# Kernel tuning notes

Hardware: AMD Instinct MI355X
Metric: run time of the kernel (lower is better)

The kernel has to match this reference:

```python
import jax, jax.numpy as jnp
import numpy as np
from jax import lax

E = 300      # _embsize
H = 32       # attention heads
ADIM = 64    # projection_dim (attention and values dim)
FF = 100     # feedforward hidden dim
NK = 11      # gaussian kernels
NCONV = 5    # conv kernel sizes 1..5
COUT = 16    # conv out channels for k>=2

def _kernel_mus(n):
    l = [1.0]
    b = 2.0 / (n - 1)
    l.append(1 - b / 2)
    for i in range(1, n - 1):
        l.append(l[i] - b)
    return l

def _kernel_sigmas(n):
    b = 2.0 / (n - 1)
    return [0.0001] + [0.5 * b] * (n - 1)

MU = jnp.asarray(_kernel_mus(NK), jnp.float32).reshape(1, 1, 1, 1, NK)
SIG = jnp.asarray(_kernel_sigmas(NK), jnp.float32).reshape(1, 1, 1, 1, NK)

def _pos_features(T, d):
    # allennlp add_positional_features, min_timescale=1, max_timescale=1e4, d even
    nt = d // 2
    inv = np.exp(np.arange(nt, dtype=np.float32) * -(np.log(1e4) / (nt - 1)))
    pos = np.arange(T, dtype=np.float32)[:, None] * inv[None, :]
    return jnp.asarray(np.concatenate([np.sin(pos), np.cos(pos)], axis=1))

def _layer_norm(x, g, b, eps=1e-6):
    m = jnp.mean(x, -1, keepdims=True)
    s = jnp.std(x, -1, keepdims=True)  # biased std, as allennlp LayerNorm
    return g * (x - m) / (s + eps) + b

def _mhsa(x, mask, Wc, bc, Wo, bo):
    # allennlp MultiHeadSelfAttention: combined projection, scale=sqrt(input_dim//heads)
    B, T, _ = x.shape
    comb = x @ Wc + bc                                   # [B,T,3*ADIM]
    q, k, v = comb[..., :ADIM], comb[..., ADIM:2 * ADIM], comb[..., 2 * ADIM:]
    dh = ADIM // H
    split = lambda t: t.reshape(B, T, H, dh).transpose(0, 2, 1, 3)
    q, k, v = split(q), split(k), split(v)
    scale = float(np.sqrt(E // H))
    sim = jnp.einsum('bhqd,bhkd->bhqk', q / scale, k)
    m = mask[:, None, None, :]
    p = jax.nn.softmax(sim * m, axis=-1) * m             # old allennlp masked_softmax
    p = p / (jnp.sum(p, -1, keepdims=True) + 1e-13)
    o = jnp.einsum('bhqk,bhkd->bhqd', p, v).transpose(0, 2, 1, 3).reshape(B, T, ADIM)
    return o @ Wo + bo

def _encode(x, mask, W1, b1, W2, b2, ffg, ffb, Wc, bc, Wo, bo, lng, lnb):
    # StackedSelfAttentionEncoder, 1 layer, all dropouts = 0
    out = x + _pos_features(x.shape[1], E)[None]
    ff = jax.nn.relu(out @ W1 + b1) @ W2 + b2
    ff = _layer_norm(ff + out, ffg, ffb)                 # residual (dims match)
    att = _mhsa(ff, mask, Wc, bc, Wo, bo)
    return _layer_norm(att + ff, lng, lnb)

def _conv(x, w, b, k):
    if k > 1:
        x = jnp.pad(x, ((0, 0), (0, 0), (0, k - 1), (0, k - 1)))  # ConstantPad2d(0,k-1,0,k-1)
    y = lax.conv_general_dilated(x, w, (1, 1), 'VALID',
                                 dimension_numbers=('NCHW', 'OIHW', 'NCHW'))
    y = y + b[None, :, None, None]
    if k > 1:
        y = jnp.max(y, axis=1, keepdims=True)            # MaxPool3d over channel dim
    return y

def setup_inputs() -> dict:
    key = jax.random.key(0)
    ks = iter(jax.random.split(key, 40))
    B, Q, D = 16, 32, 512
    nrm = lambda shape, s=0.05: jax.random.normal(next(ks), shape, jnp.float32) * s
    return {
        'query_embeddings': jax.random.normal(next(ks), (B, Q, E), jnp.float32),
        'document_embeddings': jax.random.normal(next(ks), (B, D, E), jnp.float32),
        'query_pad_oov_mask': jnp.ones((B, Q), jnp.float32),
        'document_pad_oov_mask': jnp.ones((B, D), jnp.float32),
        'query_idfs': jax.random.uniform(next(ks), (B, Q, 1), jnp.float32),
        'document_idfs': jax.random.uniform(next(ks), (B, D, 1), jnp.float32),
        'W1': nrm((E, FF)), 'b1': jnp.zeros((FF,), jnp.float32),
        'W2': nrm((FF, E)), 'b2': jnp.zeros((E,), jnp.float32),
        'ffg': jnp.ones((E,), jnp.float32), 'ffb': jnp.zeros((E,), jnp.float32),
        'Wc': nrm((E, 3 * ADIM)), 'bc': jnp.zeros((3 * ADIM,), jnp.float32),
        'Wo': nrm((ADIM, E)), 'bo': jnp.zeros((E,), jnp.float32),
        'lng': jnp.ones((E,), jnp.float32), 'lnb': jnp.zeros((E,), jnp.float32),
        'c1w': nrm((1, 2, 1, 1)), 'c1b': jnp.zeros((1,), jnp.float32),
        'c2w': nrm((COUT, 2, 2, 2)), 'c2b': jnp.zeros((COUT,), jnp.float32),
        'c3w': nrm((COUT, 2, 3, 3)), 'c3b': jnp.zeros((COUT,), jnp.float32),
        'c4w': nrm((COUT, 2, 4, 4)), 'c4b': jnp.zeros((COUT,), jnp.float32),
        'c5w': nrm((COUT, 2, 5, 5)), 'c5b': jnp.zeros((COUT,), jnp.float32),
        'dw': nrm((1, NK * NCONV)), 'db': jnp.zeros((1,), jnp.float32),
        'dmw': nrm((1, NK * NCONV)), 'dmb': jnp.zeros((1,), jnp.float32),
        'cw': nrm((1, 2)),
    }

def reference(query_embeddings, document_embeddings, query_pad_oov_mask,
              document_pad_oov_mask, query_idfs, document_idfs,
              W1, b1, W2, b2, ffg, ffb, Wc, bc, Wo, bo, lng, lnb,
              c1w, c1b, c2w, c2b, c3w, c3b, c4w, c4b, c5w, c5b,
              dw, db, dmw, dmb, cw):
    qm, dmask = query_pad_oov_mask, document_pad_oov_mask
    enc = lambda x, m: _encode(x, m, W1, b1, W2, b2, ffg, ffb, Wc, bc, Wo, bo, lng, lnb)
    q_ctx = enc(query_embeddings, qm) * qm[..., None]
    d_ctx = enc(document_embeddings, dmask) * dmask[..., None]
    # cosine on raw embeddings, dot product on contextualized
    qn = query_embeddings / (jnp.linalg.norm(query_embeddings, axis=-1, keepdims=True) + 1e-13)
    dn = document_embeddings / (jnp.linalg.norm(document_embeddings, axis=-1, keepdims=True) + 1e-13)
    cos = jnp.einsum('bqe,bde->bqd', qn, dn)[:, None]
    dot = jnp.einsum('bqe,bde->bqd', q_ctx, d_ctx)[:, None]
    combined = jnp.tanh(jnp.concatenate([cos, dot], axis=1))     # [B,2,Q,D]
    convs = [_conv(combined, w, b, k) for k, (w, b) in enumerate(
        [(c1w, c1b), (c2w, c2b), (c3w, c3b), (c4w, c4b), (c5w, c5b)], start=1)]
    all_conv = jnp.concatenate(convs, axis=1)[..., None]         # [B,5,Q,D,1]
    qd_mask = (qm[:, :, None] * dmask[:, None, :])[:, None, :, :, None]  # [B,1,Q,D,1]
    raw = jnp.exp(-(all_conv - MU) ** 2 / (2.0 * SIG ** 2))      # [B,5,Q,D,NK]
    masked = raw * qd_mask
    doc_len = jnp.sum(dmask, 1)                                  # [B]
    pkq = jnp.sum(masked, axis=3)                                # [B,5,Q,NK]
    log_pkq = jnp.log(jnp.clip(pkq, 1e-10, None)) * qm[:, None, :, None]
    per_kernel = jnp.sum(log_pkq, axis=2)                        # [B,5,NK]
    pkq_mean = pkq / doc_len[:, None, None, None]
    log_pkq_mean = jnp.log(jnp.clip(pkq_mean, 1e-10, None)) * qm[:, None, :, None]
    per_kernel_mean = jnp.sum(log_pkq_mean, axis=2)
    B = per_kernel.shape[0]
    d1 = per_kernel.reshape(B, -1) @ dw.T + db
    d2 = per_kernel_mean.reshape(B, -1) @ dmw.T + dmb
    return (jnp.concatenate([d1, d2], axis=1) @ cw.T)[:, 0]
```

## Files before the change

kernel.cpp:

```cpp
#include <hip/hip_runtime.h>

namespace {

constexpr int E_  = 300;
constexpr int FF_ = 100;
constexpr int AD_ = 64;
constexpr int NH_ = 32;
constexpr int CD_ = 192;
constexpr int B_  = 16;
constexpr int TQ_ = 32;
constexpr int TD_ = 512;
constexpr int NK_ = 11;
constexpr int DOCBLK_ = 512;

__device__ __forceinline__ float wave_sum(float v) {
#pragma unroll
  for (int o = 32; o > 0; o >>= 1) v += __shfl_down(v, o);
  return v;
}

__device__ __forceinline__ int swz16(int e, int t) {
  return e * 16 + (t ^ (((e >> 2) & 7) << 1));
}

__device__ __forceinline__ void fma4(float4& a, float s, const float4& w) {
  a.x = fmaf(s, w.x, a.x); a.y = fmaf(s, w.y, a.y);
  a.z = fmaf(s, w.z, a.z); a.w = fmaf(s, w.w, a.w);
}

__device__ __forceinline__ void gl_lds16(const float4* g, float4* l) {
  __builtin_amdgcn_global_load_lds(
      (const __attribute__((address_space(1))) void*)g,
      (__attribute__((address_space(3))) void*)l, 16, 0, 0);
}

__device__ __forceinline__ void stage_chunk(const float4* __restrict__ src,
                                            float4* __restrict__ dst,
                                            int n, int tid) {
  for (int j = tid; j < n; j += 256) gl_lds16(src + j, dst + j);
}

__global__ __launch_bounds__(256)
void encode_front_v5(const float* __restrict__ qe, const float* __restrict__ de,
                     const float* __restrict__ W1, const float* __restrict__ b1,
                     const float* __restrict__ W2, const float* __restrict__ b2,
                     const float* __restrict__ ffg, const float* __restrict__ ffb,
                     const float* __restrict__ Wc, const float* __restrict__ bc,
                     float* __restrict__ ffq, float* __restrict__ combq,
                     float* __restrict__ qn,
                     float* __restrict__ ffd, float* __restrict__ combd,
                     float* __restrict__ dnT)
{
  __shared__ float  s_A[4800];
  __shared__ float  s_h1[1600];
  __shared__ float4 s_w[2][1500];
  __shared__ float  s_stat[16][17];
  __shared__ float  s_norm[16];

  const int tid = threadIdx.x;
  const int ct = tid & 31, tg = tid >> 5;
  const int t0 = tg * 2;
  const bool doc = (blockIdx.x < DOCBLK_);
  const int sb = doc ? blockIdx.x : (blockIdx.x - DOCBLK_);
  const float* xs = (doc ? de : qe) + (size_t)sb * 16 * E_;
  float* ffo = doc ? ffd : ffq;
  float* cmo = doc ? combd : combq;
  const size_t tok0 = (size_t)sb * 16;
  const int bb_ = doc ? (int)(tok0 >> 9) : (int)(tok0 >> 5);
  const int tp0 = doc ? (int)(tok0 & 511) : (int)(tok0 & 31);

  const float4* W1f4 = (const float4*)W1;
  const float4* W2f4 = (const float4*)W2;
  const float4* Wcf4 = (const float4*)Wc;

  stage_chunk(W1f4, &s_w[0][0], 1500, tid);

  for (int i = tid; i < 1200; i += 256) {
    const float4 v = *(const float4*)(xs + (size_t)i * 4);
    const int t = i / 75, e0 = (i % 75) * 4;
    s_A[swz16(e0 + 0, t)] = v.x; s_A[swz16(e0 + 1, t)] = v.y;
    s_A[swz16(e0 + 2, t)] = v.z; s_A[swz16(e0 + 3, t)] = v.w;
  }
  __syncthreads();
  {
    const int tk = tid & 15, ch = tid >> 4;
    const int kb = ch * 19, ke = (kb + 19 < 300) ? kb + 19 : 300;
    float ss = 0.f;
    for (int k = kb; k < ke; ++k) { const float v = s_A[swz16(k, tk)]; ss = fmaf(v, v, ss); }
    s_stat[ch][tk] = ss;
  }
  __syncthreads();
  if (tid < 16) {
    float s = 0.f;
#pragma unroll
    for (int i = 0; i < 16; ++i) s += s_stat[i][tid];
    s_norm[tid] = 1.f / (sqrtf(s) + 1e-13f);
  }
  __syncthreads();
  for (int i = tid; i < 1200; i += 256) {
    const int t = i / 75, e0 = (i % 75) * 4;
    const int tp = tp0 + t;
    const float nm = s_norm[t];
#pragma unroll
    for (int j = 0; j < 4; ++j) {
      const int e = e0 + j;
      const int slot = swz16(e, t);
      const float raw = s_A[slot];
      if (doc) dnT[((size_t)bb_ * E_ + e) * 512 + tp] = raw * nm;
      else     qn[(tok0 + t) * E_ + e] = raw * nm;
      const int f = (e < 150) ? e : e - 150;
      const float ang = __expf(-0.061814365f * (float)f) * (float)tp;
      s_A[slot] = raw + ((e < 150) ? sinf(ang) : cosf(ang));
    }
  }
  __syncthreads();

  {
    const int cq = (ct < 25) ? ct : 24;
    float4 a1[2];
    a1[0] = make_float4(0.f, 0.f, 0.f, 0.f);
    a1[1] = make_float4(0.f, 0.f, 0.f, 0.f);
    for (int c = 0; c < 5; ++c) {
      if (c < 4) stage_chunk(W1f4 + 1500 * (c + 1), &s_w[(c + 1) & 1][0], 1500, tid);
      else       stage_chunk(W2f4,                  &s_w[1][0],           1500, tid);
      const float4* wb = &s_w[c & 1][0];
#pragma unroll 6
      for (int kk = 0; kk < 60; ++kk) {
        const float2 xv = *(const float2*)&s_A[swz16(c * 60 + kk, t0)];
        const float4 w = wb[kk * 25 + cq];
        fma4(a1[0], xv.x, w); fma4(a1[1], xv.y, w);
      }
      if (c == 4 && ct < 25) {
        const float4 bb = *(const float4*)&b1[4 * ct];
#pragma unroll
        for (int r = 0; r < 2; ++r) {
          const int t = t0 + r;
          const float4 a = (r == 0) ? a1[0] : a1[1];
          s_h1[swz16(4 * ct + 0, t)] = fmaxf(a.x + bb.x, 0.f);
          s_h1[swz16(4 * ct + 1, t)] = fmaxf(a.y + bb.y, 0.f);
          s_h1[swz16(4 * ct + 2, t)] = fmaxf(a.z + bb.z, 0.f);
          s_h1[swz16(4 * ct + 3, t)] = fmaxf(a.w + bb.w, 0.f);
        }
      }
      __syncthreads();
    }
  }

  {
    const int q2 = (ct < 11) ? ct + 64 : 74;
    const bool val2 = (ct < 11);
    float4 a2[3][2];
#pragma unroll
    for (int p = 0; p < 3; ++p)
#pragma unroll
      for (int r = 0; r < 2; ++r) a2[p][r] = make_float4(0.f, 0.f, 0.f, 0.f);
    for (int c = 0; c < 5; ++c) {
      if (c < 4) stage_chunk(W2f4 + 1500 * (c + 1), &s_w[c & 1][0], 1500, tid);
      else       stage_chunk(Wcf4,                  &s_w[0][0],     1440, tid);
      const float4* wb = &s_w[(c + 1) & 1][0];
#pragma unroll 5
      for (int kk = 0; kk < 20; ++kk) {
        const float2 hv = *(const float2*)&s_h1[swz16(c * 20 + kk, t0)];
        const float4 w0 = wb[kk * 75 + ct];
        const float4 w1 = wb[kk * 75 + ct + 32];
        const float4 w2 = wb[kk * 75 + q2];
        fma4(a2[0][0], hv.x, w0); fma4(a2[0][1], hv.y, w0);
        fma4(a2[1][0], hv.x, w1); fma4(a2[1][1], hv.y, w1);
        fma4(a2[2][0], hv.x, w2); fma4(a2[2][1], hv.y, w2);
      }
      if (c == 4) {
        float sum[2] = {0.f, 0.f}, sq[2] = {0.f, 0.f};
#pragma unroll
        for (int p = 0; p < 3; ++p) {
          const int qq = (p == 0) ? ct : (p == 1) ? ct + 32 : q2;
          const bool ok = (p < 2) || val2;
          if (!ok) break;
          const float4 bb = *(const float4*)&b2[4 * qq];
#pragma unroll
          for (int r = 0; r < 2; ++r) {
            const int t = t0 + r;
            float4 v = a2[p][r];
            v.x += bb.x + s_A[swz16(4 * qq + 0, t)];
            v.y += bb.y + s_A[swz16(4 * qq + 1, t)];
            v.z += bb.z + s_A[swz16(4 * qq + 2, t)];
            v.w += bb.w + s_A[swz16(4 * qq + 3, t)];
            a2[p][r] = v;
            sum[r] += v.x + v.y + v.z + v.w;
            sq[r] = fmaf(v.x, v.x, fmaf(v.y, v.y, fmaf(v.z, v.z, fmaf(v.w, v.w, sq[r]))));
          }
        }
#pragma unroll
        for (int m = 1; m <= 16; m <<= 1) {
#pragma unroll
          for (int r = 0; r < 2; ++r) {
            sum[r] += __shfl_xor(sum[r], m);
            sq[r]  += __shfl_xor(sq[r], m);
          }
        }
#pragma unroll
        for (int r = 0; r < 2; ++r) {
          const int t = t0 + r;
          const float mean = sum[r] * (1.f / 300.f);
          const float var  = fmaxf(sq[r] * (1.f / 300.f) - mean * mean, 0.f);
          const float rstd = 1.f / (sqrtf(var) + 1e-6f);
#pragma unroll
          for (int p = 0; p < 3; ++p) {
            if (p == 2 && !val2) break;
            const int qq = (p == 0) ? ct : (p == 1) ? ct + 32 : q2;
            const int c0 = 4 * qq;
            const float4 g4 = *(const float4*)&ffg[c0];
            const float4 b4 = *(const float4*)&ffb[c0];
            const float4 v = a2[p][r];
            float4 fv;
            fv.x = fmaf(g4.x, (v.x - mean) * rstd, b4.x);
            fv.y = fmaf(g4.y, (v.y - mean) * rstd, b4.y);
            fv.z = fmaf(g4.z, (v.z - mean) * rstd, b4.z);
            fv.w = fmaf(g4.w, (v.w - mean) * rstd, b4.w);
            *(float4*)&ffo[(tok0 + t) * E_ + c0] = fv;
            s_A[swz16(c0 + 0, t)] = fv.x; s_A[swz16(c0 + 1, t)] = fv.y;
            s_A[swz16(c0 + 2, t)] = fv.z; s_A[swz16(c0 + 3, t)] = fv.w;
          }
        }
      }
      __syncthreads();
    }
  }

  {
    const int q3 = (ct < 16) ? ct + 32 : 47;
    float4 a3[2][2];
#pragma unroll
    for (int p = 0; p < 2; ++p)
#pragma unroll
      for (int r = 0; r < 2; ++r) a3[p][r] = make_float4(0.f, 0.f, 0.f, 0.f);
    for (int c = 0; c < 10; ++c) {
      if (c < 9) stage_chunk(Wcf4 + 1440 * (c + 1), &s_w[(c + 1) & 1][0], 1440, tid);
      const float4* wb = &s_w[c & 1][0];
#pragma unroll 6
      for (int kk = 0; kk < 30; ++kk) {
        const float2 xv = *(const float2*)&s_A[swz16(c * 30 + kk, t0)];
        const float4 w0 = wb[kk * 48 + ct];
        const float4 w1 = wb[kk * 48 + q3];
        fma4(a3[0][0], xv.x, w0); fma4(a3[0][1], xv.y, w0);
        fma4(a3[1][0], xv.x, w1); fma4(a3[1][1], xv.y, w1);
      }
      if (c < 9) __syncthreads();
    }
    const float4 bb0 = *(const float4*)&bc[4 * ct];
#pragma unroll
    for (int r = 0; r < 2; ++r) {
      float4 o = a3[0][r];
      o.x += bb0.x; o.y += bb0.y; o.z += bb0.z; o.w += bb0.w;
      *(float4*)&cmo[(tok0 + t0 + r) * CD_ + 4 * ct] = o;
    }
    if (ct < 16) {
      const float4 bb1 = *(const float4*)&bc[4 * (ct + 32)];
#pragma unroll
      for (int r = 0; r < 2; ++r) {
        float4 o = a3[1][r];
        o.x += bb1.x; o.y += bb1.y; o.z += bb1.z; o.w += bb1.w;
        *(float4*)&cmo[(tok0 + t0 + r) * CD_ + 4 * (ct + 32)] = o;
      }
    }
  }
}

template <int T>
__global__ __launch_bounds__(512)
void attn(const float* __restrict__ comb, const float* __restrict__ mask,
          float* __restrict__ o)
{
  __shared__ float4 s_kv[T];
  __shared__ float  s_m[T];
  const int bh = blockIdx.x, b = bh / NH_, h = bh % NH_;
  const int tid = threadIdx.x;
  const float* cb = comb + (size_t)b * T * CD_;
  if (tid < T) {
    const float* c = cb + (size_t)tid * CD_;
    const float m = mask[b * T + tid];
    s_kv[tid] = make_float4(c[AD_ + 2 * h] * m, c[AD_ + 2 * h + 1] * m,
                            c[2 * AD_ + 2 * h], c[2 * AD_ + 2 * h + 1]);
    s_m[tid] = m;
  }
  __syncthreads();
  if (tid < T) {
    const float* c = cb + (size_t)tid * CD_;
    const float q0 = c[2 * h] * (1.f / 3.f);
    const float q1 = c[2 * h + 1] * (1.f / 3.f);
    float M = -1e30f;
    for (int j = 0; j < T; ++j) {
      const float4 kv = s_kv[j];
      M = fmaxf(M, fmaf(q0, kv.x, q1 * kv.y));
    }
    float S = 0.f, W = 0.f, a0 = 0.f, a1 = 0.f;
    for (int j = 0; j < T; ++j) {
      const float4 kv = s_kv[j];
      const float s = fmaf(q0, kv.x, q1 * kv.y);
      const float z = __expf(s - M);
      const float w = z * s_m[j];
      S += z; W += w;
      a0 = fmaf(w, kv.z, a0);
      a1 = fmaf(w, kv.w, a1);
    }
    const float dn = 1.f / (W + 1e-13f * S);
    float* op = o + (size_t)(b * T + tid) * AD_ + 2 * h;
    op[0] = a0 * dn;
    op[1] = a1 * dn;
  }
}

__global__ __launch_bounds__(256)
void encode_back_v3(const float* __restrict__ oq, const float* __restrict__ od,
                    const float* __restrict__ ffq, const float* __restrict__ ffd,
                    const float* __restrict__ Wo, const float* __restrict__ bo,
                    const float* __restrict__ lng, const float* __restrict__ lnb,
                    const float* __restrict__ qm, const float* __restrict__ dm,
                    float* __restrict__ qctx, float* __restrict__ dctxT)
{
  __shared__ float  s_O[1024];
  __shared__ float4 s_w[2][1200];

  const int tid = threadIdx.x;
  const int ct = tid & 31, tg = tid >> 5;
  const int t0 = tg * 2;
  const bool doc = (blockIdx.x < DOCBLK_);
  const int sb = doc ? blockIdx.x : (blockIdx.x - DOCBLK_);
  const size_t tok0 = (size_t)sb * 16;
  const float* op = doc ? od : oq;
  const float* ffp = doc ? ffd : ffq;
  const float* mp = doc ? dm : qm;
  const int bb_ = doc ? (int)(tok0 >> 9) : 0;
  const int tp0 = doc ? (int)(tok0 & 511) : 0;

  const float4* Wof4 = (const float4*)Wo;
  stage_chunk(Wof4, &s_w[0][0], 1200, tid);

  {
    const int t = tid >> 4, c0 = (tid & 15) * 4;
    const float4 v = *(const float4*)(op + (tok0 + t) * AD_ + c0);
    s_O[swz16(c0 + 0, t)] = v.x; s_O[swz16(c0 + 1, t)] = v.y;
    s_O[swz16(c0 + 2, t)] = v.z; s_O[swz16(c0 + 3, t)] = v.w;
  }
  __syncthreads();

  const int q2 = (ct < 11) ? ct + 64 : 74;
  const bool val2 = (ct < 11);
  float4 a[3][2];
#pragma unroll
  for (int p = 0; p < 3; ++p)
#pragma unroll
    for (int r = 0; r < 2; ++r) a[p][r] = make_float4(0.f, 0.f, 0.f, 0.f);
  for (int c = 0; c < 4; ++c) {
    if (c < 3) stage_chunk(Wof4 + 1200 * (c + 1), &s_w[(c + 1) & 1][0], 1200, tid);
    const float4* wb = &s_w[c & 1][0];
#pragma unroll 4
    for (int kk = 0; kk < 16; ++kk) {
      const float2 ov = *(const float2*)&s_O[swz16(c * 16 + kk, t0)];
      const float4 w0 = wb[kk * 75 + ct];
      const float4 w1 = wb[kk * 75 + ct + 32];
      const float4 w2 = wb[kk * 75 + q2];
      fma4(a[0][0], ov.x, w0); fma4(a[0][1], ov.y, w0);
      fma4(a[1][0], ov.x, w1); fma4(a[1][1], ov.y, w1);
      fma4(a[2][0], ov.x, w2); fma4(a[2][1], ov.y, w2);
    }
    if (c < 3) __syncthreads();
  }
  float sum[2] = {0.f, 0.f}, sq[2] = {0.f, 0.f};
#pragma unroll
  for (int p = 0; p < 3; ++p) {
    const int qq = (p == 0) ? ct : (p == 1) ? ct + 32 : q2;
    const bool ok = (p < 2) || val2;
    if (!ok) break;
    const float4 bb = *(const float4*)&bo[4 * qq];
#pragma unroll
    for (int r = 0; r < 2; ++r) {
      const int t = t0 + r;
      const float4 f4 = *(const float4*)(ffp + (tok0 + t) * E_ + 4 * qq);
      float4 v = a[p][r];
      v.x += bb.x + f4.x; v.y += bb.y + f4.y;
      v.z += bb.z + f4.z; v.w += bb.w + f4.w;
      a[p][r] = v;
      sum[r] += v.x + v.y + v.z + v.w;
      sq[r] = fmaf(v.x, v.x, fmaf(v.y, v.y, fmaf(v.z, v.z, fmaf(v.w, v.w, sq[r]))));
    }
  }
#pragma unroll
  for (int m = 1; m <= 16; m <<= 1) {
#pragma unroll
    for (int r = 0; r < 2; ++r) {
      sum[r] += __shfl_xor(sum[r], m);
      sq[r]  += __shfl_xor(sq[r], m);
    }
  }
#pragma unroll
  for (int r = 0; r < 2; ++r) {
    const int t = t0 + r;
    const float mean = sum[r] * (1.f / 300.f);
    const float var  = fmaxf(sq[r] * (1.f / 300.f) - mean * mean, 0.f);
    const float rstd = 1.f / (sqrtf(var) + 1e-6f);
    const float mk = mp[tok0 + t];
#pragma unroll
    for (int p = 0; p < 3; ++p) {
      if (p == 2 && !val2) break;
      const int qq = (p == 0) ? ct : (p == 1) ? ct + 32 : q2;
      const int c0 = 4 * qq;
      const float4 g4 = *(const float4*)&lng[c0];
      const float4 b4 = *(const float4*)&lnb[c0];
      const float4 v = a[p][r];
      float4 fv;
      fv.x = fmaf(g4.x, (v.x - mean) * rstd, b4.x) * mk;
      fv.y = fmaf(g4.y, (v.y - mean) * rstd, b4.y) * mk;
      fv.z = fmaf(g4.z, (v.z - mean) * rstd, b4.z) * mk;
      fv.w = fmaf(g4.w, (v.w - mean) * rstd, b4.w) * mk;
      if (doc) {
        const int tp = tp0 + t;
        dctxT[((size_t)bb_ * E_ + c0 + 0) * 512 + tp] = fv.x;
        dctxT[((size_t)bb_ * E_ + c0 + 1) * 512 + tp] = fv.y;
        dctxT[((size_t)bb_ * E_ + c0 + 2) * 512 + tp] = fv.z;
        dctxT[((size_t)bb_ * E_ + c0 + 3) * 512 + tp] = fv.w;
      } else {
        *(float4*)&qctx[(tok0 + t) * E_ + c0] = fv;
      }
    }
  }
}

__global__ __launch_bounds__(512)
void simtanh_v2(const float* __restrict__ qctx, const float* __restrict__ qn,
                const float* __restrict__ dctxT, const float* __restrict__ dnT,
                float* __restrict__ combined)
{
  __shared__ float s_q[2 * 16 * 304];
  __shared__ float s_part[8 * 32 * 64];

  const int bid = blockIdx.x;
  const int sub = bid & 15, b = bid >> 4;
  const int qh = sub >> 3, dc = sub & 7;
  const int tid = threadIdx.x;
  const int ep = tid >> 6, dlane = tid & 63;
  const int d = dc * 64 + dlane;

  const float* qc  = qctx + ((size_t)b * 32 + qh * 16) * E_;
  const float* qnp = qn   + ((size_t)b * 32 + qh * 16) * E_;
  for (int i = tid; i < 1200; i += 512) {
    const int q = i / 75, e0 = (i % 75) * 4;
    *(float4*)&s_q[(0 * 16 + q) * 304 + e0] = *(const float4*)(qc + q * E_ + e0);
    *(float4*)&s_q[(1 * 16 + q) * 304 + e0] = *(const float4*)(qnp + q * E_ + e0);
  }
  __syncthreads();

  const float* dct = dctxT + (size_t)b * E_ * 512 + d;
  const float* dnt = dnT   + (size_t)b * E_ * 512 + d;
  float accD[16], accC[16];
#pragma unroll
  for (int q = 0; q < 16; ++q) { accD[q] = 0.f; accC[q] = 0.f; }
  const int es = ep * 40, ee = (es + 40 < 300) ? es + 40 : 300;
  for (int e0 = es; e0 < ee; e0 += 4) {
    const float dv0 = dct[(size_t)(e0 + 0) * 512];
    const float dv1 = dct[(size_t)(e0 + 1) * 512];
    const float dv2 = dct[(size_t)(e0 + 2) * 512];
    const float dv3 = dct[(size_t)(e0 + 3) * 512];
    const float dn0 = dnt[(size_t)(e0 + 0) * 512];
    const float dn1 = dnt[(size_t)(e0 + 1) * 512];
    const float dn2 = dnt[(size_t)(e0 + 2) * 512];
    const float dn3 = dnt[(size_t)(e0 + 3) * 512];
#pragma unroll
    for (int q = 0; q < 16; ++q) {
      const float4 qd = *(const float4*)&s_q[(0 * 16 + q) * 304 + e0];
      const float4 qc4 = *(const float4*)&s_q[(1 * 16 + q) * 304 + e0];
      float aD = accD[q], aC = accC[q];
      aD = fmaf(qd.x, dv0, aD); aD = fmaf(qd.y, dv1, aD);
      aD = fmaf(qd.z, dv2, aD); aD = fmaf(qd.w, dv3, aD);
      aC = fmaf(qc4.x, dn0, aC); aC = fmaf(qc4.y, dn1, aC);
      aC = fmaf(qc4.z, dn2, aC); aC = fmaf(qc4.w, dn3, aC);
      accD[q] = aD; accC[q] = aC;
    }
  }
#pragma unroll
  for (int q = 0; q < 16; ++q) {
    s_part[(ep * 32 + q * 2 + 0) * 64 + dlane] = accC[q];
    s_part[(ep * 32 + q * 2 + 1) * 64 + dlane] = accD[q];
  }
  __syncthreads();
  const int s0 = (tid >> 6) * 4;
#pragma unroll
  for (int si = 0; si < 4; ++si) {
    const int s = s0 + si;
    float v = 0.f;
#pragma unroll
    for (int p = 0; p < 8; ++p) v += s_part[(p * 32 + s) * 64 + dlane];
    const int q = s >> 1, typ = s & 1;
    combined[(((size_t)b * 2 + typ) * 32 + qh * 16 + q) * 512 + d] = tanhf(v);
  }
}

template <int K>
__device__ __forceinline__ float conv_max16(const float* __restrict__ s_in, int j,
                                            const float* __restrict__ w,
                                            const float* __restrict__ bias)
{
  float patch[2][K][K];
#pragma unroll
  for (int c = 0; c < 2; ++c)
#pragma unroll
    for (int di = 0; di < K; ++di)
#pragma unroll
      for (int dj = 0; dj < K; ++dj)
        patch[c][di][dj] = s_in[(c * 5 + di) * 516 + j + dj];
  float best = -1e30f;
#pragma unroll
  for (int oc = 0; oc < 16; ++oc) {
    float acc = bias[oc];
#pragma unroll
    for (int c = 0; c < 2; ++c)
#pragma unroll
      for (int di = 0; di < K; ++di)
#pragma unroll
        for (int dj = 0; dj < K; ++dj)
          acc = fmaf(patch[c][di][dj], w[((oc * 2 + c) * K + di) * K + dj], acc);
    best = fmaxf(best, acc);
  }
  return best;
}

__global__ __launch_bounds__(512)
void conv_all(const float* __restrict__ combined,
              const float* __restrict__ c1w, const float* __restrict__ c1b,
              const float* __restrict__ c2w, const float* __restrict__ c2b,
              const float* __restrict__ c3w, const float* __restrict__ c3b,
              const float* __restrict__ c4w, const float* __restrict__ c4b,
              const float* __restrict__ c5w, const float* __restrict__ c5b,
              float* __restrict__ convout)
{
  __shared__ float s_in[2 * 5 * 516];
  __shared__ float s_w[1730];
  __shared__ float s_b[66];
  const int blk = blockIdx.x, b = blk >> 5, i = blk & 31;
  const int tid = threadIdx.x;
  for (int idx = tid; idx < 2 * 5 * 516; idx += 512) {
    const int c = idx / (5 * 516), rem = idx % (5 * 516), r = rem / 516, j = rem % 516;
    const int row = i + r;
    float v = 0.f;
    if (row < 32 && j < 512)
      v = combined[((size_t)(b * 2 + c) * 32 + row) * 512 + j];
    s_in[idx] = v;
  }
  if (tid < 2)   s_w[tid] = c1w[tid];
  if (tid < 128) s_w[2 + tid] = c2w[tid];
  if (tid < 288) s_w[130 + tid] = c3w[tid];
  s_w[418 + tid] = c4w[tid];
  for (int idx = tid; idx < 800; idx += 512) s_w[930 + idx] = c5w[idx];
  if (tid == 0) s_b[0] = c1b[0];
  if (tid < 16) {
    s_b[1 + tid]  = c2b[tid];
    s_b[17 + tid] = c3b[tid];
    s_b[33 + tid] = c4b[tid];
    s_b[49 + tid] = c5b[tid];
  }
  __syncthreads();
  const int j = tid;
  const float o1 = fmaf(s_in[j], s_w[0], fmaf(s_in[5 * 516 + j], s_w[1], s_b[0]));
  convout[((size_t)(b * 5 + 0) * 32 + i) * 512 + j] = o1;
  convout[((size_t)(b * 5 + 1) * 32 + i) * 512 + j] = conv_max16<2>(s_in, j, s_w + 2,   s_b + 1);
  convout[((size_t)(b * 5 + 2) * 32 + i) * 512 + j] = conv_max16<3>(s_in, j, s_w + 130, s_b + 17);
  convout[((size_t)(b * 5 + 3) * 32 + i) * 512 + j] = conv_max16<4>(s_in, j, s_w + 418, s_b + 33);
  convout[((size_t)(b * 5 + 4) * 32 + i) * 512 + j] = conv_max16<5>(s_in, j, s_w + 930, s_b + 49);
}

__global__ __launch_bounds__(512)
void rbf_pkq(const float* __restrict__ convout, const float* __restrict__ dmask,
             const float* __restrict__ qmask, float* __restrict__ pkq)
{
  __shared__ float red[8][NK_];
  const int id = blockIdx.x;
  const int q = id & 31;
  const int b = id / 160;
  const int tid = threadIdx.x;
  const float x = convout[(size_t)id * 512 + tid];
  const float dmv = dmask[b * 512 + tid];
  const float mu[NK_]  = {1.f, .9f, .7f, .5f, .3f, .1f, -.1f, -.3f, -.5f, -.7f, -.9f};
  const float nis[NK_] = {-5e7f, -50.f, -50.f, -50.f, -50.f, -50.f,
                          -50.f, -50.f, -50.f, -50.f, -50.f};
  const int lane = tid & 63, w = tid >> 6;
#pragma unroll
  for (int k = 0; k < NK_; ++k) {
    const float df = x - mu[k];
    float v = __expf(df * df * nis[k]) * dmv;
    v = wave_sum(v);
    if (lane == 0) red[w][k] = v;
  }
  __syncthreads();
  if (tid < NK_) {
    float s = 0.f;
#pragma unroll
    for (int ww = 0; ww < 8; ++ww) s += red[ww][tid];
    pkq[(size_t)id * NK_ + tid] = s * qmask[b * 32 + q];
  }
}

__global__ __launch_bounds__(64)
void final_k(const float* __restrict__ pkq, const float* __restrict__ qmask,
             const float* __restrict__ dmask,
             const float* __restrict__ dw, const float* __restrict__ db,
             const float* __restrict__ dmw, const float* __restrict__ dmb,
             const float* __restrict__ cw, float* __restrict__ out)
{
  const int b = blockIdx.x, tid = threadIdx.x;
  float dl = 0.f;
  for (int j = tid; j < 512; j += 64) dl += dmask[b * 512 + j];
  dl = wave_sum(dl);
  dl = __shfl(dl, 0);
  float v1 = 0.f, v2 = 0.f;
  if (tid < 55) {
    const int c = tid / NK_, k = tid % NK_;
    const float rdl = 1.f / dl;
    float s1 = 0.f, s2 = 0.f;
    for (int q = 0; q < 32; ++q) {
      const float p = pkq[(size_t)((b * 5 + c) * 32 + q) * NK_ + k];
      const float qmv = qmask[b * 32 + q];
      s1 += logf(fmaxf(p, 1e-10f)) * qmv;
      s2 += logf(fmaxf(p * rdl, 1e-10f)) * qmv;
    }
    v1 = s1 * dw[tid];
    v2 = s2 * dmw[tid];
  }
  v1 = wave_sum(v1);
  v2 = wave_sum(v2);
  if (tid == 0) out[b] = (v1 + db[0]) * cw[0] + (v2 + dmb[0]) * cw[1];
}

}

extern "C" void kernel_launch(void* const* d_in, const int* in_sizes, int n_in,
                              void* d_out, int out_size, void* d_ws, size_t ws_size,
                              hipStream_t stream)
{
  const float* qe  = (const float*)d_in[0];
  const float* de  = (const float*)d_in[1];
  const float* qm  = (const float*)d_in[2];
  const float* dm  = (const float*)d_in[3];
  const float* W1  = (const float*)d_in[6];
  const float* b1  = (const float*)d_in[7];
  const float* W2  = (const float*)d_in[8];
  const float* b2  = (const float*)d_in[9];
  const float* ffg = (const float*)d_in[10];
  const float* ffb = (const float*)d_in[11];
  const float* Wc  = (const float*)d_in[12];
  const float* bc  = (const float*)d_in[13];
  const float* Wo  = (const float*)d_in[14];
  const float* bo  = (const float*)d_in[15];
  const float* lng = (const float*)d_in[16];
  const float* lnb = (const float*)d_in[17];
  const float* c1w = (const float*)d_in[18];
  const float* c1b = (const float*)d_in[19];
  const float* c2w = (const float*)d_in[20];
  const float* c2b = (const float*)d_in[21];
  const float* c3w = (const float*)d_in[22];
  const float* c3b = (const float*)d_in[23];
  const float* c4w = (const float*)d_in[24];
  const float* c4b = (const float*)d_in[25];
  const float* c5w = (const float*)d_in[26];
  const float* c5b = (const float*)d_in[27];
  const float* dwp  = (const float*)d_in[28];
  const float* dbp  = (const float*)d_in[29];
  const float* dmwp = (const float*)d_in[30];
  const float* dmbp = (const float*)d_in[31];
  const float* cwp  = (const float*)d_in[32];

  float* ws = (float*)d_ws;
  size_t off = 0;
  auto alloc = [&](size_t n) { float* p = ws + off; off += n; return p; };
  float* ffq      = alloc((size_t)B_ * TQ_ * E_);
  float* combq    = alloc((size_t)B_ * TQ_ * CD_);
  float* oq       = alloc((size_t)B_ * TQ_ * AD_);
  float* qctx     = alloc((size_t)B_ * TQ_ * E_);
  float* qn       = alloc((size_t)B_ * TQ_ * E_);
  float* ffd      = alloc((size_t)B_ * TD_ * E_);
  float* combd    = alloc((size_t)B_ * TD_ * CD_);
  float* od       = alloc((size_t)B_ * TD_ * AD_);
  float* dctxT    = alloc((size_t)B_ * E_ * TD_);
  float* dnT      = alloc((size_t)B_ * E_ * TD_);
  float* combined = alloc((size_t)B_ * 2 * TQ_ * TD_);
  float* convout  = alloc((size_t)B_ * 5 * TQ_ * TD_);
  float* pkq      = alloc((size_t)B_ * 5 * TQ_ * NK_);

  encode_front_v5<<<DOCBLK_ + 32, 256, 0, stream>>>(
      qe, de, W1, b1, W2, b2, ffg, ffb, Wc, bc,
      ffq, combq, qn, ffd, combd, dnT);
  attn<TQ_><<<B_ * NH_, 64, 0, stream>>>(combq, qm, oq);
  attn<TD_><<<B_ * NH_, 512, 0, stream>>>(combd, dm, od);
  encode_back_v3<<<DOCBLK_ + 32, 256, 0, stream>>>(
      oq, od, ffq, ffd, Wo, bo, lng, lnb, qm, dm, qctx, dctxT);
  simtanh_v2<<<256, 512, 0, stream>>>(qctx, qn, dctxT, dnT, combined);
  conv_all<<<B_ * 32, 512, 0, stream>>>(
      combined, c1w, c1b, c2w, c2b, c3w, c3b, c4w, c4b, c5w, c5b, convout);
  rbf_pkq<<<B_ * 5 * TQ_, 512, 0, stream>>>(convout, dm, qm, pkq);
  final_k<<<B_, 64, 0, stream>>>(pkq, qm, dm, dwp, dbp, dmwp, dmbp, cwp,
                                 (float*)d_out);
}
```

Measured before the change: 382.0 us.

## Read encoder weights directly from global memory instead of LDS double-buffering

Removes the global_load_lds double-buffered staging of W1, W2, Wc and Wo in the encode front and back kernels. Weight rows are now read straight from global memory (through the caches) inside single flat k-loops, with no per-chunk barriers. This cuts LDS usage per block, which can raise occupancy, and drops many __syncthreads, but each thread now waits on global/L2 latency for weights that used to be prefetched.

After: 415.8 us. 8.8% more time.

```diff
diff --git a/kernel.cpp b/kernel.cpp
--- a/kernel.cpp
+++ b/kernel.cpp
@@ -28,20 +28,8 @@
   a.z = fmaf(s, w.z, a.z); a.w = fmaf(s, w.w, a.w);
 }
 
-__device__ __forceinline__ void gl_lds16(const float4* g, float4* l) {
-  __builtin_amdgcn_global_load_lds(
-      (const __attribute__((address_space(1))) void*)g,
-      (__attribute__((address_space(3))) void*)l, 16, 0, 0);
-}
-
-__device__ __forceinline__ void stage_chunk(const float4* __restrict__ src,
-                                            float4* __restrict__ dst,
-                                            int n, int tid) {
-  for (int j = tid; j < n; j += 256) gl_lds16(src + j, dst + j);
-}
-
 __global__ __launch_bounds__(256)
-void encode_front_v5(const float* __restrict__ qe, const float* __restrict__ de,
+void encode_front_v6(const float* __restrict__ qe, const float* __restrict__ de,
                      const float* __restrict__ W1, const float* __restrict__ b1,
                      const float* __restrict__ W2, const float* __restrict__ b2,
                      const float* __restrict__ ffg, const float* __restrict__ ffb,
@@ -51,11 +39,10 @@
                      float* __restrict__ ffd, float* __restrict__ combd,
                      float* __restrict__ dnT)
 {
-  __shared__ float  s_A[4800];
-  __shared__ float  s_h1[1600];
-  __shared__ float4 s_w[2][1500];
-  __shared__ float  s_stat[16][17];
-  __shared__ float  s_norm[16];
+  __shared__ float s_A[4800];
+  __shared__ float s_h1[1600];
+  __shared__ float s_stat[16][17];
+  __shared__ float s_norm[16];
 
   const int tid = threadIdx.x;
   const int ct = tid & 31, tg = tid >> 5;
@@ -73,8 +60,6 @@
   const float4* W2f4 = (const float4*)W2;
   const float4* Wcf4 = (const float4*)Wc;
 
-  stage_chunk(W1f4, &s_w[0][0], 1500, tid);
-
   for (int i = tid; i < 1200; i += 256) {
     const float4 v = *(const float4*)(xs + (size_t)i * 4);
     const int t = i / 75, e0 = (i % 75) * 4;
@@ -120,30 +105,25 @@
     float4 a1[2];
     a1[0] = make_float4(0.f, 0.f, 0.f, 0.f);
     a1[1] = make_float4(0.f, 0.f, 0.f, 0.f);
-    for (int c = 0; c < 5; ++c) {
-      if (c < 4) stage_chunk(W1f4 + 1500 * (c + 1), &s_w[(c + 1) & 1][0], 1500, tid);
-      else       stage_chunk(W2f4,                  &s_w[1][0],           1500, tid);
-      const float4* wb = &s_w[c & 1][0];
-#pragma unroll 6
-      for (int kk = 0; kk < 60; ++kk) {
-        const float2 xv = *(const float2*)&s_A[swz16(c * 60 + kk, t0)];
-        const float4 w = wb[kk * 25 + cq];
-        fma4(a1[0], xv.x, w); fma4(a1[1], xv.y, w);
+#pragma unroll 10
+    for (int k = 0; k < 300; ++k) {
+      const float2 xv = *(const float2*)&s_A[swz16(k, t0)];
+      const float4 w = W1f4[k * 25 + cq];
+      fma4(a1[0], xv.x, w); fma4(a1[1], xv.y, w);
+    }
+    if (ct < 25) {
+      const float4 bb = *(const float4*)&b1[4 * ct];
+#pragma unroll
+      for (int r = 0; r < 2; ++r) {
+        const int t = t0 + r;
+        const float4 a = (r == 0) ? a1[0] : a1[1];
+        s_h1[swz16(4 * ct + 0, t)] = fmaxf(a.x + bb.x, 0.f);
+        s_h1[swz16(4 * ct + 1, t)] = fmaxf(a.y + bb.y, 0.f);
+        s_h1[swz16(4 * ct + 2, t)] = fmaxf(a.z + bb.z, 0.f);
+        s_h1[swz16(4 * ct + 3, t)] = fmaxf(a.w + bb.w, 0.f);
       }
-      if (c == 4 && ct < 25) {
-        const float4 bb = *(const float4*)&b1[4 * ct];
-#pragma unroll
-        for (int r = 0; r < 2; ++r) {
-          const int t = t0 + r;
-          const float4 a = (r == 0) ? a1[0] : a1[1];
-          s_h1[swz16(4 * ct + 0, t)] = fmaxf(a.x + bb.x, 0.f);
-          s_h1[swz16(4 * ct + 1, t)] = fmaxf(a.y + bb.y, 0.f);
-          s_h1[swz16(4 * ct + 2, t)] = fmaxf(a.z + bb.z, 0.f);
-          s_h1[swz16(4 * ct + 3, t)] = fmaxf(a.w + bb.w, 0.f);
-        }
-      }
-      __syncthreads();
-    }
+    }
+    __syncthreads();
   }
 
   {
@@ -154,76 +134,69 @@
     for (int p = 0; p < 3; ++p)
 #pragma unroll
       for (int r = 0; r < 2; ++r) a2[p][r] = make_float4(0.f, 0.f, 0.f, 0.f);
-    for (int c = 0; c < 5; ++c) {
-      if (c < 4) stage_chunk(W2f4 + 1500 * (c + 1), &s_w[c & 1][0], 1500, tid);
-      else       stage_chunk(Wcf4,                  &s_w[0][0],     1440, tid);
-      const float4* wb = &s_w[(c + 1) & 1][0];
 #pragma unroll 5
-      for (int kk = 0; kk < 20; ++kk) {
-        const float2 hv = *(const float2*)&s_h1[swz16(c * 20 + kk, t0)];
-        const float4 w0 = wb[kk * 75 + ct];
-        const float4 w1 = wb[kk * 75 + ct + 32];
-        const float4 w2 = wb[kk * 75 + q2];
-        fma4(a2[0][0], hv.x, w0); fma4(a2[0][1], hv.y, w0);
-        fma4(a2[1][0], hv.x, w1); fma4(a2[1][1], hv.y, w1);
-        fma4(a2[2][0], hv.x, w2); fma4(a2[2][1], hv.y, w2);
+    for (int k = 0; k < 100; ++k) {
+      const float2 hv = *(const float2*)&s_h1[swz16(k, t0)];
+      const float4 w0 = W2f4[k * 75 + ct];
+      const float4 w1 = W2f4[k * 75 + ct + 32];
+      const float4 w2 = W2f4[k * 75 + q2];
+      fma4(a2[0][0], hv.x, w0); fma4(a2[0][1], hv.y, w0);
+      fma4(a2[1][0], hv.x, w1); fma4(a2[1][1], hv.y, w1);
+      fma4(a2[2][0], hv.x, w2); fma4(a2[2][1], hv.y, w2);
+    }
+    float sum[2] = {0.f, 0.f}, sq[2] = {0.f, 0.f};
+#pragma unroll
+    for (int p = 0; p < 3; ++p) {
+      const int qq = (p == 0) ? ct : (p == 1) ? ct + 32 : q2;
+      const bool ok = (p < 2) || val2;
+      if (!ok) break;
+      const float4 bb = *(const float4*)&b2[4 * qq];
+#pragma unroll
+      for (int r = 0; r < 2; ++r) {
+        const int t = t0 + r;
+        float4 v = a2[p][r];
+        v.x += bb.x + s_A[swz16(4 * qq + 0, t)];
+        v.y += bb.y + s_A[swz16(4 * qq + 1, t)];
+        v.z += bb.z + s_A[swz16(4 * qq + 2, t)];
+        v.w += bb.w + s_A[swz16(4 * qq + 3, t)];
+        a2[p][r] = v;
+        sum[r] += v.x + v.y + v.z + v.w;
+        sq[r] = fmaf(v.x, v.x, fmaf(v.y, v.y, fmaf(v.z, v.z, fmaf(v.w, v.w, sq[r]))));
       }
-      if (c == 4) {
-        float sum[2] = {0.f, 0.f}, sq[2] = {0.f, 0.f};
-#pragma unroll
-        for (int p = 0; p < 3; ++p) {
-          const int qq = (p == 0) ? ct : (p == 1) ? ct + 32 : q2;
-          const bool ok = (p < 2) || val2;
-          if (!ok) break;
-          const float4 bb = *(const float4*)&b2[4 * qq];
-#pragma unroll
-          for (int r = 0; r < 2; ++r) {
-            const int t = t0 + r;
-            float4 v = a2[p][r];
-            v.x += bb.x + s_A[swz16(4 * qq + 0, t)];
-            v.y += bb.y + s_A[swz16(4 * qq + 1, t)];
-            v.z += bb.z + s_A[swz16(4 * qq + 2, t)];
-            v.w += bb.w + s_A[swz16(4 * qq + 3, t)];
-            a2[p][r] = v;
-            sum[r] += v.x + v.y + v.z + v.w;
-            sq[r] = fmaf(v.x, v.x, fmaf(v.y, v.y, fmaf(v.z, v.z, fmaf(v.w, v.w, sq[r]))));
-          }
-        }
-#pragma unroll
-        for (int m = 1; m <= 16; m <<= 1) {
-#pragma unroll
-          for (int r = 0; r < 2; ++r) {
-            sum[r] += __shfl_xor(sum[r], m);
-            sq[r]  += __shfl_xor(sq[r], m);
-          }
-        }
-#pragma unroll
-        for (int r = 0; r < 2; ++r) {
-          const int t = t0 + r;
-          const float mean = sum[r] * (1.f / 300.f);
-          const float var  = fmaxf(sq[r] * (1.f / 300.f) - mean * mean, 0.f);
-          const float rstd = 1.f / (sqrtf(var) + 1e-6f);
-#pragma unroll
-          for (int p = 0; p < 3; ++p) {
-            if (p == 2 && !val2) break;
-            const int qq = (p == 0) ? ct : (p == 1) ? ct + 32 : q2;
-            const int c0 = 4 * qq;
-            const float4 g4 = *(const float4*)&ffg[c0];
-            const float4 b4 = *(const float4*)&ffb[c0];
-            const float4 v = a2[p][r];
-            float4 fv;
-            fv.x = fmaf(g4.x, (v.x - mean) * rstd, b4.x);
-            fv.y = fmaf(g4.y, (v.y - mean) * rstd, b4.y);
-            fv.z = fmaf(g4.z, (v.z - mean) * rstd, b4.z);
-            fv.w = fmaf(g4.w, (v.w - mean) * rstd, b4.w);
-            *(float4*)&ffo[(tok0 + t) * E_ + c0] = fv;
-            s_A[swz16(c0 + 0, t)] = fv.x; s_A[swz16(c0 + 1, t)] = fv.y;
-            s_A[swz16(c0 + 2, t)] = fv.z; s_A[swz16(c0 + 3, t)] = fv.w;
-          }
-        }
+    }
+#pragma unroll
+    for (int m = 1; m <= 16; m <<= 1) {
+#pragma unroll
+      for (int r = 0; r < 2; ++r) {
+        sum[r] += __shfl_xor(sum[r], m);
+        sq[r]  += __shfl_xor(sq[r], m);
       }
-      __syncthreads();
-    }
+    }
+#pragma unroll
+    for (int r = 0; r < 2; ++r) {
+      const int t = t0 + r;
+      const float mean = sum[r] * (1.f / 300.f);
+      const float var  = fmaxf(sq[r] * (1.f / 300.f) - mean * mean, 0.f);
+      const float rstd = 1.f / (sqrtf(var) + 1e-6f);
+#pragma unroll
+      for (int p = 0; p < 3; ++p) {
+        if (p == 2 && !val2) break;
+        const int qq = (p == 0) ? ct : (p == 1) ? ct + 32 : q2;
+        const int c0 = 4 * qq;
+        const float4 g4 = *(const float4*)&ffg[c0];
+        const float4 b4 = *(const float4*)&ffb[c0];
+        const float4 v = a2[p][r];
+        float4 fv;
+        fv.x = fmaf(g4.x, (v.x - mean) * rstd, b4.x);
+        fv.y = fmaf(g4.y, (v.y - mean) * rstd, b4.y);
+        fv.z = fmaf(g4.z, (v.z - mean) * rstd, b4.z);
+        fv.w = fmaf(g4.w, (v.w - mean) * rstd, b4.w);
+        *(float4*)&ffo[(tok0 + t) * E_ + c0] = fv;
+        s_A[swz16(c0 + 0, t)] = fv.x; s_A[swz16(c0 + 1, t)] = fv.y;
+        s_A[swz16(c0 + 2, t)] = fv.z; s_A[swz16(c0 + 3, t)] = fv.w;
+      }
+    }
+    __syncthreads();
   }
 
   {
@@ -233,18 +206,13 @@
     for (int p = 0; p < 2; ++p)
 #pragma unroll
       for (int r = 0; r < 2; ++r) a3[p][r] = make_float4(0.f, 0.f, 0.f, 0.f);
-    for (int c = 0; c < 10; ++c) {
-      if (c < 9) stage_chunk(Wcf4 + 1440 * (c + 1), &s_w[(c + 1) & 1][0], 1440, tid);
-      const float4* wb = &s_w[c & 1][0];
-#pragma unroll 6
-      for (int kk = 0; kk < 30; ++kk) {
-        const float2 xv = *(const float2*)&s_A[swz16(c * 30 + kk, t0)];
-        const float4 w0 = wb[kk * 48 + ct];
-        const float4 w1 = wb[kk * 48 + q3];
-        fma4(a3[0][0], xv.x, w0); fma4(a3[0][1], xv.y, w0);
-        fma4(a3[1][0], xv.x, w1); fma4(a3[1][1], xv.y, w1);
-      }
-      if (c < 9) __syncthreads();
+#pragma unroll 10
+    for (int k = 0; k < 300; ++k) {
+      const float2 xv = *(const float2*)&s_A[swz16(k, t0)];
+      const float4 w0 = Wcf4[k * 48 + ct];
+      const float4 w1 = Wcf4[k * 48 + q3];
+      fma4(a3[0][0], xv.x, w0); fma4(a3[0][1], xv.y, w0);
+      fma4(a3[1][0], xv.x, w1); fma4(a3[1][1], xv.y, w1);
     }
     const float4 bb0 = *(const float4*)&bc[4 * ct];
 #pragma unroll
@@ -310,15 +278,14 @@
 }
 
 __global__ __launch_bounds__(256)
-void encode_back_v3(const float* __restrict__ oq, const float* __restrict__ od,
+void encode_back_v4(const float* __restrict__ oq, const float* __restrict__ od,
                     const float* __restrict__ ffq, const float* __restrict__ ffd,
                     const float* __restrict__ Wo, const float* __restrict__ bo,
                     const float* __restrict__ lng, const float* __restrict__ lnb,
                     const float* __restrict__ qm, const float* __restrict__ dm,
                     float* __restrict__ qctx, float* __restrict__ dctxT)
 {
-  __shared__ float  s_O[1024];
-  __shared__ float4 s_w[2][1200];
+  __shared__ float s_O[1024];
 
   const int tid = threadIdx.x;
   const int ct = tid & 31, tg = tid >> 5;
@@ -333,7 +300,6 @@
   const int tp0 = doc ? (int)(tok0 & 511) : 0;
 
   const float4* Wof4 = (const float4*)Wo;
-  stage_chunk(Wof4, &s_w[0][0], 1200, tid);
 
   {
     const int t = tid >> 4, c0 = (tid & 15) * 4;
@@ -350,20 +316,15 @@
   for (int p = 0; p < 3; ++p)
 #pragma unroll
     for (int r = 0; r < 2; ++r) a[p][r] = make_float4(0.f, 0.f, 0.f, 0.f);
-  for (int c = 0; c < 4; ++c) {
-    if (c < 3) stage_chunk(Wof4 + 1200 * (c + 1), &s_w[(c + 1) & 1][0], 1200, tid);
-    const float4* wb = &s_w[c & 1][0];
-#pragma unroll 4
-    for (int kk = 0; kk < 16; ++kk) {
-      const float2 ov = *(const float2*)&s_O[swz16(c * 16 + kk, t0)];
-      const float4 w0 = wb[kk * 75 + ct];
-      const float4 w1 = wb[kk * 75 + ct + 32];
-      const float4 w2 = wb[kk * 75 + q2];
-      fma4(a[0][0], ov.x, w0); fma4(a[0][1], ov.y, w0);
-      fma4(a[1][0], ov.x, w1); fma4(a[1][1], ov.y, w1);
-      fma4(a[2][0], ov.x, w2); fma4(a[2][1], ov.y, w2);
-    }
-    if (c < 3) __syncthreads();
+#pragma unroll 8
+  for (int k = 0; k < 64; ++k) {
+    const float2 ov = *(const float2*)&s_O[swz16(k, t0)];
+    const float4 w0 = Wof4[k * 75 + ct];
+    const float4 w1 = Wof4[k * 75 + ct + 32];
+    const float4 w2 = Wof4[k * 75 + q2];
+    fma4(a[0][0], ov.x, w0); fma4(a[0][1], ov.y, w0);
+    fma4(a[1][0], ov.x, w1); fma4(a[1][1], ov.y, w1);
+    fma4(a[2][0], ov.x, w2); fma4(a[2][1], ov.y, w2);
   }
   float sum[2] = {0.f, 0.f}, sq[2] = {0.f, 0.f};
 #pragma unroll
@@ -684,12 +645,12 @@
   float* convout  = alloc((size_t)B_ * 5 * TQ_ * TD_);
   float* pkq      = alloc((size_t)B_ * 5 * TQ_ * NK_);
 
-  encode_front_v5<<<DOCBLK_ + 32, 256, 0, stream>>>(
+  encode_front_v6<<<DOCBLK_ + 32, 256, 0, stream>>>(
       qe, de, W1, b1, W2, b2, ffg, ffb, Wc, bc,
       ffq, combq, qn, ffd, combd, dnT);
   attn<TQ_><<<B_ * NH_, 64, 0, stream>>>(combq, qm, oq);
   attn<TD_><<<B_ * NH_, 512, 0, stream>>>(combd, dm, od);
-  encode_back_v3<<<DOCBLK_ + 32, 256, 0, stream>>>(
+  encode_back_v4<<<DOCBLK_ + 32, 256, 0, stream>>>(
       oq, od, ffq, ffd, Wo, bo, lng, lnb, qm, dm, qctx, dctxT);
   simtanh_v2<<<256, 512, 0, stream>>>(qctx, qn, dctxT, dnT, combined);
   conv_all<<<B_ * 32, 512, 0, stream>>>(
```
